# Kernel tuning notes

Hardware: AMD Instinct MI355X
Metric: run time of the kernel (lower is better)

## Reference

```python
import jax, jax.numpy as jnp
import numpy as np

KH, KW = 7, 7      # t2t kernel_size
ST = 3             # stride
PD = 3             # padding
K = KH * KW        # 49 taps per patch


def _patch_indices(H, W):
    """Linear indices into the padded (Hp,Wp) image for every (patch l, tap k)."""
    Hp, Wp = H + 2 * PD, W + 2 * PD
    oh = (H + 2 * PD - KH) // ST + 1
    ow = (W + 2 * PD - KW) // ST + 1
    ki, kj = np.meshgrid(np.arange(KH), np.arange(KW), indexing='ij')
    rows = (np.arange(oh) * ST)[:, None, None, None] + ki[None, None]   # (oh,1,kh,kw)
    cols = (np.arange(ow) * ST)[None, :, None, None] + kj[None, None]   # (1,ow,kh,kw)
    idx = (rows * Wp + cols).reshape(oh * ow, K)                        # (L, 49)
    return jnp.asarray(idx), Hp, Wp, oh * ow


def setup_inputs() -> dict:
    key = jax.random.key(0)
    k1, k2, k3 = jax.random.split(key, 3)
    b, n, d, hd = 2, 5760, 512, 1960
    return {
        'x': jax.random.normal(k1, (b, n, d), dtype=jnp.float32),
        'W1': jax.random.normal(k2, (d, hd), dtype=jnp.float32) * 0.02,
        'b1': jnp.zeros((hd,), dtype=jnp.float32),
        'W2': jax.random.normal(k3, (hd, d), dtype=jnp.float32) * 0.02,
        'b2': jnp.zeros((d,), dtype=jnp.float32),
        'out_h': 60,
        'out_w': 108,
    }


def reference(x, W1, b1, W2, b2, out_h, out_w):
    H, W = int(out_h), int(out_w)
    idx, Hp, Wp, L = _patch_indices(H, W)          # idx: (L, 49)
    idxf = idx.reshape(-1)                         # (L*49,)

    b, n, _ = x.shape
    h = x @ W1 + b1                                # (b, n, 1960)
    hd = h.shape[-1]
    C = hd // K                                    # 40 fold channels
    Bp = (b * n) // L                              # fold batch (= b * t)

    # fold input layout: (Bp, C, K, L) -> scatter-add into padded image
    patches = h.reshape(Bp, L, C, K)
    vals = jnp.transpose(patches, (0, 2, 1, 3)).reshape(Bp * C, L * K)
    img = jnp.zeros((Bp * C, Hp * Wp), x.dtype).at[:, idxf].add(vals)

    # overlap-count normalizer (fold of ones), same for every batch/channel
    count = jnp.zeros((Hp * Wp,), x.dtype).at[idxf].add(jnp.ones_like(idxf, x.dtype))

    # crop padding (as F.fold does), normalize, re-pad with zeros (as F.unfold does)
    img = img.reshape(Bp, C, Hp, Wp)[:, :, PD:PD + H, PD:PD + W]
    cnt = count.reshape(Hp, Wp)[PD:PD + H, PD:PD + W]
    img = img / cnt
    flat = jnp.pad(img, ((0, 0), (0, 0), (PD, PD), (PD, PD))).reshape(Bp * C, Hp * Wp)

    # unfold: gather the same taps back, restore (b, n, hd) token layout
    g = flat[:, idxf].reshape(Bp, C, L, K)
    g = jnp.transpose(g, (0, 2, 1, 3)).reshape(b, n, hd)

    return jax.nn.gelu(g, approximate=False) @ W2 + b2
```

## Files before the change

### kernel.cpp

```cpp
#include <hip/hip_runtime.h>

typedef _Float16 f16;
typedef __attribute__((ext_vector_type(8))) _Float16 half8;
typedef __attribute__((ext_vector_type(4))) _Float16 half4;
typedef __attribute__((ext_vector_type(4))) float f32x4;

#define LDS_AS __attribute__((address_space(3)))
#define GLB_AS __attribute__((address_space(1)))

__device__ __forceinline__ void load16_lds(const f16* g, f16* l) {
    __builtin_amdgcn_global_load_lds((GLB_AS void*)(g), (LDS_AS void*)(l), 16, 0, 0);
}

#define WAIT4_BARRIER()  asm volatile("s_waitcnt vmcnt(4)\n\ts_barrier" ::: "memory")
#define WAIT3_BARRIER()  asm volatile("s_waitcnt vmcnt(3)\n\ts_barrier" ::: "memory")
#define WAIT0_BARRIER()  asm volatile("s_waitcnt vmcnt(0)\n\ts_barrier" ::: "memory")
#define PLAIN_BARRIER()  asm volatile("s_barrier" ::: "memory")

__global__ __launch_bounds__(256, 3) void gemm1(
    const f16* __restrict__ A, const f16* __restrict__ Bt,
    const float* __restrict__ bias, f16* __restrict__ C)
{
    const int id  = blockIdx.x;
    const int xcd = id & 7;
    const int r   = id >> 3;
    const int mt  = r & 15;
    const int nt  = xcd + 8 * (r >> 4);
    if (nt >= 90) return;
    const int m0 = mt * 128, n0 = nt * 128;
    const int K = 512, ldc = 11520;

    __shared__ f16 As[2][128 * 32];
    __shared__ f16 Bs[2][128 * 32];
    const int tid  = threadIdx.x;
    const int wave = tid >> 6;
    const int lane = tid & 63;

    const int s0 = tid, s1 = tid + 256;
    const f16* gA0 = A  + (m0 + (s0 >> 2)) * K + (s0 & 3) * 8;
    const f16* gA1 = A  + (m0 + (s1 >> 2)) * K + (s1 & 3) * 8;
    const f16* gB0 = Bt + (n0 + (s0 >> 2)) * K + (s0 & 3) * 8;
    const f16* gB1 = Bt + (n0 + (s1 >> 2)) * K + (s1 & 3) * 8;

    const int wm = (wave >> 1) * 64;
    const int wn = (wave & 1) * 64;
    const int lr = lane & 15;
    const int k8 = (lane >> 4) * 8;

    f32x4 acc[4][4];
#pragma unroll
    for (int i = 0; i < 4; ++i)
#pragma unroll
        for (int j = 0; j < 4; ++j) acc[i][j] = f32x4{0.f, 0.f, 0.f, 0.f};

#define G1_ISSUE(st, k0) do { \
    load16_lds(gA0 + (k0), &As[st][wave * 512]); \
    load16_lds(gA1 + (k0), &As[st][2048 + wave * 512]); \
    load16_lds(gB0 + (k0), &Bs[st][wave * 512]); \
    load16_lds(gB1 + (k0), &Bs[st][2048 + wave * 512]); \
} while (0)

    G1_ISSUE(0, 0);
    const int NS = 16;
    for (int s = 0; s < NS; ++s) {
        const int cur = s & 1;
        if (s + 1 < NS) {
            G1_ISSUE(cur ^ 1, (s + 1) * 32);
            WAIT4_BARRIER();
        } else {
            WAIT0_BARRIER();
        }
        half8 af[4], bf[4];
#pragma unroll
        for (int i = 0; i < 4; ++i)
            af[i] = *(const half8*)&As[cur][(wm + i * 16 + lr) * 32 + k8];
#pragma unroll
        for (int j = 0; j < 4; ++j)
            bf[j] = *(const half8*)&Bs[cur][(wn + j * 16 + lr) * 32 + k8];
#pragma unroll
        for (int i = 0; i < 4; ++i)
#pragma unroll
            for (int j = 0; j < 4; ++j)
                acc[i][j] = __builtin_amdgcn_mfma_f32_16x16x32_f16(
                    af[i], bf[j], acc[i][j], 0, 0, 0);
        PLAIN_BARRIER();
    }

#pragma unroll
    for (int i = 0; i < 4; ++i) {
#pragma unroll
        for (int rr = 0; rr < 4; ++rr) {
            const int row = m0 + wm + i * 16 + (lane >> 4) * 4 + rr;
            const float bvr = (row < 1960) ? bias[row] : 0.f;
#pragma unroll
            for (int j = 0; j < 4; ++j) {
                const int col = n0 + wn + j * 16 + lr;
                C[row * ldc + col] = (f16)(acc[i][j][rr] + bvr);
            }
        }
    }
}

__global__ __launch_bounds__(512, 4) void gemm2(
    const f16* __restrict__ A, const f16* __restrict__ Bt,
    const float* __restrict__ bias, float* __restrict__ Cout)
{
    const int id = blockIdx.x;
    const int nt = id / 96;
    const int mt = id % 96;
    if (mt >= 90) return;
    const int m0 = mt * 128, n0 = nt * 64;

    __shared__ f16 smem[24576];
    const int tid  = threadIdx.x;
    const int half = tid >> 8;
    const int t    = tid & 255;
    const int wave = (tid >> 6) & 3;
    const int lane = tid & 63;

    const int kbase = half * 1024;
    const int s1 = t + 256;
    const f16* gA0 = A  + (m0 + (t  >> 2)) * 2048 + kbase + (t  & 3) * 8;
    const f16* gA1 = A  + (m0 + (s1 >> 2)) * 2048 + kbase + (s1 & 3) * 8;
    const f16* gB0 = Bt + (n0 + (t  >> 2)) * 2048 + kbase + (t  & 3) * 8;
    f16* hb = &smem[half * 12288];

    const int wm = (wave >> 1) * 64;
    const int wn = (wave & 1) * 32;
    const int lr = lane & 15;
    const int k8 = (lane >> 4) * 8;

    f32x4 acc[4][2];
#pragma unroll
    for (int i = 0; i < 4; ++i)
#pragma unroll
        for (int j = 0; j < 2; ++j) acc[i][j] = f32x4{0.f, 0.f, 0.f, 0.f};

#define G2_ISSUE(st, k0) do { \
    f16* sb = hb + (st) * 6144; \
    load16_lds(gA0 + (k0), sb + wave * 512); \
    load16_lds(gA1 + (k0), sb + 2048 + wave * 512); \
    load16_lds(gB0 + (k0), sb + 4096 + wave * 512); \
} while (0)

    G2_ISSUE(0, 0);
    const int NS = 32;
    for (int s = 0; s < NS; ++s) {
        const int cur = s & 1;
        if (s + 1 < NS) {
            G2_ISSUE(cur ^ 1, (s + 1) * 32);
            WAIT3_BARRIER();
        } else {
            WAIT0_BARRIER();
        }
        const f16* sa = hb + cur * 6144;
        half8 af[4], bf[2];
#pragma unroll
        for (int i = 0; i < 4; ++i)
            af[i] = *(const half8*)&sa[(wm + i * 16 + lr) * 32 + k8];
#pragma unroll
        for (int j = 0; j < 2; ++j)
            bf[j] = *(const half8*)&sa[4096 + (wn + j * 16 + lr) * 32 + k8];
#pragma unroll
        for (int i = 0; i < 4; ++i)
#pragma unroll
            for (int j = 0; j < 2; ++j)
                acc[i][j] = __builtin_amdgcn_mfma_f32_16x16x32_f16(
                    af[i], bf[j], acc[i][j], 0, 0, 0);
        PLAIN_BARRIER();
    }

    float* accl = (float*)smem;
    if (half == 1) {
#pragma unroll
        for (int i = 0; i < 4; ++i)
#pragma unroll
            for (int rr = 0; rr < 4; ++rr) {
                const int row = wm + i * 16 + (lane >> 4) * 4 + rr;
#pragma unroll
                for (int j = 0; j < 2; ++j)
                    accl[row * 64 + wn + j * 16 + lr] = acc[i][j][rr];
            }
    }
    __syncthreads();
    if (half == 0) {
#pragma unroll
        for (int j = 0; j < 2; ++j) {
            const int col = wn + j * 16 + lr;
            const float bv = bias[n0 + col];
#pragma unroll
            for (int i = 0; i < 4; ++i) {
#pragma unroll
                for (int rr = 0; rr < 4; ++rr) {
                    const int row = wm + i * 16 + (lane >> 4) * 4 + rr;
                    Cout[(m0 + row) * 512 + n0 + col] =
                        acc[i][j][rr] + accl[row * 64 + col] + bv;
                }
            }
        }
    }
}

__global__ void fold_gelu(const f16* __restrict__ h_t, f16* __restrict__ imgG)
{
    const int r  = blockIdx.x;
    const int bc = blockIdx.y;
    const int bp  = bc / 40;
    const int cch = bc % 40;
    const int c = threadIdx.x;
    if (c >= 114) return;
    float outv = 0.f;
    if (r >= 3 && r < 63 && c >= 3 && c < 111) {
        const int qr = r / 3, rm = r % 3;
        const int qc = c / 3, cm = c % 3;
        int kis[3], ohs[3], nr = 0;
        int kjs[3], ows[3], nc = 0;
#pragma unroll
        for (int t = 0; t < 3; ++t) {
            const int ki = rm + 3 * t, oh = qr - t;
            if (ki < 7 && oh >= 0 && oh < 20) { kis[nr] = ki; ohs[nr] = oh; ++nr; }
            const int kj = cm + 3 * t, ow = qc - t;
            if (kj < 7 && ow >= 0 && ow < 36) { kjs[nc] = kj; ows[nc] = ow; ++nc; }
        }
        float sum = 0.f;
        for (int a = 0; a < nr; ++a)
            for (int b = 0; b < nc; ++b) {
                const int n = cch * 49 + kis[a] * 7 + kjs[b];
                const int token = bp * 720 + ohs[a] * 36 + ows[b];
                sum += (float)h_t[n * 11520 + token];
            }
        const float xv = sum / (float)(nr * nc);
        outv = 0.5f * xv * (1.f + erff(xv * 0.70710678118654752f));
    }
    imgG[(bc * 66 + r) * 114 + c] = (f16)outv;
}

__global__ __launch_bounds__(256) void unfold_lds(
    const f16* __restrict__ imgG, f16* __restrict__ g16)
{
    __shared__ f16 ch[7524];
    const int bc = blockIdx.x;
    const int bp = bc / 40, cch = bc % 40;
    const float* src = (const float*)(imgG + bc * 7524);
    float* dst = (float*)ch;
    for (int i = threadIdx.x; i < 3762; i += 256) dst[i] = src[i];
    __syncthreads();
    const int tokbase = bp * 720;
    const int colbase = cch * 49;
    for (int flat = threadIdx.x; flat < 35280; flat += 256) {
        const int l = flat / 49, k = flat - l * 49;
        const int oh = l / 36, ow = l - oh * 36;
        const int ki = k / 7,  kj = k - ki * 7;
        g16[(tokbase + l) * 2048 + colbase + k] =
            ch[(oh * 3 + ki) * 114 + ow * 3 + kj];
    }
    if (cch >= 36) {
        const int cb = 1960 + (cch - 36) * 22;
        for (int flat = threadIdx.x; flat < 720 * 22; flat += 256) {
            const int l = flat / 22, k = flat - l * 22;
            g16[(tokbase + l) * 2048 + cb + k] = (f16)0.f;
        }
    }
}

__global__ __launch_bounds__(256) void prep(
    const float* __restrict__ x, f16* __restrict__ xh,
    const float* __restrict__ W1, f16* __restrict__ W1t,
    const float* __restrict__ W2, f16* __restrict__ W2t)
{
    __shared__ float tile[32][33];
    const int b = blockIdx.x, t = threadIdx.x;
    if (b < 5760) {
        const int i = b * 256 + t;
        const float4 v = ((const float4*)x)[i];
        half4 o;
        o[0] = (f16)v.x; o[1] = (f16)v.y; o[2] = (f16)v.z; o[3] = (f16)v.w;
        ((half4*)xh)[i] = o;
        return;
    }
    const float* src; f16* dst; int R, C, Rp, Cp, bx, by;
    if (b < 6784) {
        const int local = b - 5760;
        bx = local & 15; by = local >> 4;
        src = W1; dst = W1t; R = 512; C = 1960; Rp = 512; Cp = 2048;
    } else {
        const int local = b - 6784;
        bx = local & 63; by = local >> 6;
        src = W2; dst = W2t; R = 1960; C = 512; Rp = 2048; Cp = 512;
    }
    const int r0 = bx * 32, c0 = by * 32;
    const int tx = t & 31, ty = t >> 5;
#pragma unroll
    for (int i = 0; i < 32; i += 8) {
        const int r = r0 + ty + i, c = c0 + tx;
        tile[ty + i][tx] = (r < R && c < C) ? src[r * C + c] : 0.f;
    }
    __syncthreads();
#pragma unroll
    for (int i = 0; i < 32; i += 8) {
        const int c = c0 + ty + i, r = r0 + tx;
        if (c < Cp && r < Rp) dst[c * Rp + r] = (f16)tile[tx][ty + i];
    }
}

extern "C" void kernel_launch(void* const* d_in, const int* in_sizes, int n_in,
                              void* d_out, int out_size, void* d_ws, size_t ws_size,
                              hipStream_t stream)
{
    const float* x  = (const float*)d_in[0];
    const float* W1 = (const float*)d_in[1];
    const float* b1 = (const float*)d_in[2];
    const float* W2 = (const float*)d_in[3];
    const float* b2 = (const float*)d_in[4];

    char* ws = (char*)d_ws;
    f16* xh   = (f16*)(ws);
    f16* W1t  = (f16*)(ws + 11796480);
    f16* W2t  = (f16*)(ws + 11796480 + 2097152);
    f16* hbuf = (f16*)(ws + 11796480 + 2 * 2097152);
    f16* imgG = (f16*)(ws + 11796480 + 2 * 2097152 + 47185920);

    prep<<<dim3(7808), dim3(256), 0, stream>>>(x, xh, W1, W1t, W2, W2t);
    gemm1<<<dim3(1536), dim3(256), 0, stream>>>(W1t, xh, b1, hbuf);
    fold_gelu<<<dim3(66, 640), dim3(128), 0, stream>>>(hbuf, imgG);
    unfold_lds<<<dim3(640), dim3(256), 0, stream>>>(imgG, hbuf);
    gemm2<<<dim3(768), dim3(512), 0, stream>>>(hbuf, W2t, b2, (float*)d_out);
}
```

Before: 233.0 us.

## Restructure gemm2 as 128x128 tiles with triple-buffered full-K pipeline

gemm2 drops the split-K design, where two 256-thread halves each covered half of K and were reduced through LDS. Each 256-thread block now computes a full 128x128 output tile over all of K, using a three-stage global-to-LDS prefetch ring and an XCD-aware block mapping. The intent is more operand reuse per block and removal of the LDS reduction epilogue. In exchange, each block runs a longer serial K loop, occupancy drops, and only 360 active blocks remain. The end-of-iteration barrier in both GEMMs now also waits on lgkmcnt before reusing buffers.

Measured after the change: 226.9 us. 2.6% less time.

```diff
diff --git a/kernel.cpp b/kernel.cpp
--- a/kernel.cpp
+++ b/kernel.cpp
@@ -12,10 +12,10 @@
     __builtin_amdgcn_global_load_lds((GLB_AS void*)(g), (LDS_AS void*)(l), 16, 0, 0);
 }
 
+#define WAIT8_BARRIER()  asm volatile("s_waitcnt vmcnt(8)\n\ts_barrier" ::: "memory")
 #define WAIT4_BARRIER()  asm volatile("s_waitcnt vmcnt(4)\n\ts_barrier" ::: "memory")
-#define WAIT3_BARRIER()  asm volatile("s_waitcnt vmcnt(3)\n\ts_barrier" ::: "memory")
 #define WAIT0_BARRIER()  asm volatile("s_waitcnt vmcnt(0)\n\ts_barrier" ::: "memory")
-#define PLAIN_BARRIER()  asm volatile("s_barrier" ::: "memory")
+#define ENDBAR()         asm volatile("s_waitcnt lgkmcnt(0)\n\ts_barrier" ::: "memory")
 
 __global__ __launch_bounds__(256, 3) void gemm1(
     const f16* __restrict__ A, const f16* __restrict__ Bt,
@@ -83,7 +83,7 @@
             for (int j = 0; j < 4; ++j)
                 acc[i][j] = __builtin_amdgcn_mfma_f32_16x16x32_f16(
                     af[i], bf[j], acc[i][j], 0, 0, 0);
-        PLAIN_BARRIER();
+        ENDBAR();
     }
 
 #pragma unroll
@@ -101,102 +101,89 @@
     }
 }
 
-__global__ __launch_bounds__(512, 4) void gemm2(
+__global__ __launch_bounds__(256, 2) void gemm2(
     const f16* __restrict__ A, const f16* __restrict__ Bt,
     const float* __restrict__ bias, float* __restrict__ Cout)
 {
-    const int id = blockIdx.x;
-    const int nt = id / 96;
-    const int mt = id % 96;
+    const int id  = blockIdx.x;
+    const int xcd = id & 7;
+    const int j2  = id >> 3;
+    const int nt  = j2 & 3;
+    const int mt  = (j2 >> 2) * 8 + xcd;
     if (mt >= 90) return;
-    const int m0 = mt * 128, n0 = nt * 64;
+    const int m0 = mt * 128, n0 = nt * 128;
 
     __shared__ f16 smem[24576];
     const int tid  = threadIdx.x;
-    const int half = tid >> 8;
-    const int t    = tid & 255;
-    const int wave = (tid >> 6) & 3;
+    const int wave = tid >> 6;
     const int lane = tid & 63;
 
-    const int kbase = half * 1024;
-    const int s1 = t + 256;
-    const f16* gA0 = A  + (m0 + (t  >> 2)) * 2048 + kbase + (t  & 3) * 8;
-    const f16* gA1 = A  + (m0 + (s1 >> 2)) * 2048 + kbase + (s1 & 3) * 8;
-    const f16* gB0 = Bt + (n0 + (t  >> 2)) * 2048 + kbase + (t  & 3) * 8;
-    f16* hb = &smem[half * 12288];
+    const int s1 = tid + 256;
+    const f16* gA0 = A  + (m0 + (tid >> 2)) * 2048 + (tid & 3) * 8;
+    const f16* gA1 = A  + (m0 + (s1 >> 2)) * 2048 + (s1 & 3) * 8;
+    const f16* gB0 = Bt + (n0 + (tid >> 2)) * 2048 + (tid & 3) * 8;
+    const f16* gB1 = Bt + (n0 + (s1 >> 2)) * 2048 + (s1 & 3) * 8;
 
     const int wm = (wave >> 1) * 64;
-    const int wn = (wave & 1) * 32;
+    const int wn = (wave & 1) * 64;
     const int lr = lane & 15;
     const int k8 = (lane >> 4) * 8;
 
-    f32x4 acc[4][2];
+    f32x4 acc[4][4];
 #pragma unroll
     for (int i = 0; i < 4; ++i)
 #pragma unroll
-        for (int j = 0; j < 2; ++j) acc[i][j] = f32x4{0.f, 0.f, 0.f, 0.f};
+        for (int j = 0; j < 4; ++j) acc[i][j] = f32x4{0.f, 0.f, 0.f, 0.f};
 
 #define G2_ISSUE(st, k0) do { \
-    f16* sb = hb + (st) * 6144; \
-    load16_lds(gA0 + (k0), sb + wave * 512); \
-    load16_lds(gA1 + (k0), sb + 2048 + wave * 512); \
-    load16_lds(gB0 + (k0), sb + 4096 + wave * 512); \
+    f16* sb_ = &smem[(st) * 8192]; \
+    load16_lds(gA0 + (k0), sb_ + wave * 512); \
+    load16_lds(gA1 + (k0), sb_ + 2048 + wave * 512); \
+    load16_lds(gB0 + (k0), sb_ + 4096 + wave * 512); \
+    load16_lds(gB1 + (k0), sb_ + 6144 + wave * 512); \
 } while (0)
 
     G2_ISSUE(0, 0);
-    const int NS = 32;
+    G2_ISSUE(1, 32);
+    const int NS = 64;
+    int cur = 0;
     for (int s = 0; s < NS; ++s) {
-        const int cur = s & 1;
-        if (s + 1 < NS) {
-            G2_ISSUE(cur ^ 1, (s + 1) * 32);
-            WAIT3_BARRIER();
-        } else {
-            WAIT0_BARRIER();
-        }
-        const f16* sa = hb + cur * 6144;
-        half8 af[4], bf[2];
+        if (s + 2 < NS) {
+            int pre = cur + 2; if (pre >= 3) pre -= 3;
+            G2_ISSUE(pre, (s + 2) * 32);
+        }
+        const int rem = NS - 1 - s;
+        if (rem >= 2)      WAIT8_BARRIER();
+        else if (rem == 1) WAIT4_BARRIER();
+        else               WAIT0_BARRIER();
+        const f16* sa = &smem[cur * 8192];
+        half8 af[4], bf[4];
 #pragma unroll
         for (int i = 0; i < 4; ++i)
             af[i] = *(const half8*)&sa[(wm + i * 16 + lr) * 32 + k8];
 #pragma unroll
-        for (int j = 0; j < 2; ++j)
+        for (int j = 0; j < 4; ++j)
             bf[j] = *(const half8*)&sa[4096 + (wn + j * 16 + lr) * 32 + k8];
 #pragma unroll
         for (int i = 0; i < 4; ++i)
 #pragma unroll
-            for (int j = 0; j < 2; ++j)
+            for (int j = 0; j < 4; ++j)
                 acc[i][j] = __builtin_amdgcn_mfma_f32_16x16x32_f16(
                     af[i], bf[j], acc[i][j], 0, 0, 0);
-        PLAIN_BARRIER();
-    }
-
-    float* accl = (float*)smem;
-    if (half == 1) {
-#pragma unroll
-        for (int i = 0; i < 4; ++i)
-#pragma unroll
-            for (int rr = 0; rr < 4; ++rr) {
-                const int row = wm + i * 16 + (lane >> 4) * 4 + rr;
-#pragma unroll
-                for (int j = 0; j < 2; ++j)
-                    accl[row * 64 + wn + j * 16 + lr] = acc[i][j][rr];
-            }
-    }
-    __syncthreads();
-    if (half == 0) {
-#pragma unroll
-        for (int j = 0; j < 2; ++j) {
-            const int col = wn + j * 16 + lr;
-            const float bv = bias[n0 + col];
-#pragma unroll
-            for (int i = 0; i < 4; ++i) {
-#pragma unroll
-                for (int rr = 0; rr < 4; ++rr) {
-                    const int row = wm + i * 16 + (lane >> 4) * 4 + rr;
-                    Cout[(m0 + row) * 512 + n0 + col] =
-                        acc[i][j][rr] + accl[row * 64 + col] + bv;
-                }
-            }
+        ENDBAR();
+        ++cur; if (cur >= 3) cur = 0;
+    }
+
+#pragma unroll
+    for (int j = 0; j < 4; ++j) {
+        const int col = n0 + wn + j * 16 + lr;
+        const float bv = bias[col];
+#pragma unroll
+        for (int i = 0; i < 4; ++i) {
+            const int rbase = m0 + wm + i * 16 + (lane >> 4) * 4;
+#pragma unroll
+            for (int rr = 0; rr < 4; ++rr)
+                Cout[(rbase + rr) * 512 + col] = acc[i][j][rr] + bv;
         }
     }
 }
@@ -324,5 +311,5 @@
     gemm1<<<dim3(1536), dim3(256), 0, stream>>>(W1t, xh, b1, hbuf);
     fold_gelu<<<dim3(66, 640), dim3(128), 0, stream>>>(hbuf, imgG);
     unfold_lds<<<dim3(640), dim3(256), 0, stream>>>(imgG, hbuf);
-    gemm2<<<dim3(768), dim3(512), 0, stream>>>(hbuf, W2t, b2, (float*)d_out);
-}
+    gemm2<<<dim3(384), dim3(256), 0, stream>>>(hbuf, W2t, b2, (float*)d_out);
+}
```
